# Performance work log

Measured on AMD Instinct MI355X. Metric: run time of the kernel, lower is better.

The kernel has to match this reference:

```python
import jax, jax.numpy as jnp
import numpy as np

N_IN, N_OUT, K, G = 128, 256, 3, 3  # G = grid intervals (setup hard-codes 3)
KNOT_LO, KNOT_HI = -1.0, 1.0


def make_grid(n, k, G, lo=KNOT_LO, hi=KNOT_HI):
    # Augmented knot vector: G+1 knots extended by k on each side -> G+2k+1 points
    h = (hi - lo) / G
    g = jnp.arange(-k, G + k + 1, dtype=jnp.float32) * h + lo
    return jnp.tile(g[None, :], (n, 1))  # (n, G+2k+1)


def get_spline_basis(x, grid, k):
    # Cox-de Boor recursion. x: (batch, n); grid: (n, G+2k+1)
    g = grid[None, :, :]          # (1, n, G+2k+1)
    xx = x[:, :, None]            # (batch, n, 1)
    # order-0 (indicator) basis: (batch, n, G+2k)
    basis = ((xx >= g[..., :-1]) & (xx < g[..., 1:])).astype(x.dtype)
    for kk in range(1, k + 1):
        left = (xx - g[..., : -(kk + 1)]) / (g[..., kk:-1] - g[..., : -(kk + 1)]) * basis[..., :-1]
        right = (g[..., kk + 1 :] - xx) / (g[..., kk + 1 :] - g[..., 1:-kk]) * basis[..., 1:]
        basis = left + right
    return basis  # (batch, n, G+k)


def setup_inputs() -> dict:
    key = jax.random.key(0)
    k1, k2 = jax.random.split(key)
    batch = 512
    n = N_IN * N_OUT
    x = jax.random.normal(k1, (batch, N_IN), dtype=jnp.float32)
    grid = make_grid(n, K, G)                                        # state (non-trainable)
    c_basis = 0.1 * jax.random.normal(k2, (n, G + K), dtype=jnp.float32)
    c_spl = jnp.ones((n,), dtype=jnp.float32)
    c_res = jnp.ones((n,), dtype=jnp.float32)
    return {"x": x, "grid": grid, "c_basis": c_basis, "c_spl": c_spl, "c_res": c_res}


def reference(x, grid, c_basis, c_spl, c_res):
    batch = x.shape[0]
    # Broadcast each input node to every output edge, out-major ordering:
    # einsum('ij,k->ikj', x, ones(n_out)).reshape(batch, n_in*n_out)
    x_ext = jnp.broadcast_to(x[:, None, :], (batch, N_OUT, N_IN)).reshape(batch, N_OUT * N_IN)
    # residual branch: swish, transposed to (n, batch)
    res = jax.nn.swish(x_ext).T
    # spline branch: (batch, n, G+K) basis combined with per-edge coeffs -> (n, batch)
    Bi = get_spline_basis(x_ext, grid, K)
    spl = jnp.einsum('ij,bij->ib', c_basis, Bi)
    y = c_spl[:, None] * spl + c_res[:, None] * res            # (n, batch)
    y = y.reshape(N_OUT, N_IN, batch).sum(axis=1) / N_IN       # (n_out, batch)
    return y.T                                                 # (batch, n_out)
```

## Files before the change

### kernel.cpp

```cpp
#include <hip/hip_runtime.h>
#include <hip/hip_bf16.h>


typedef short short8 __attribute__((ext_vector_type(8)));
typedef float f32x4 __attribute__((ext_vector_type(4)));

static __device__ inline unsigned short bf16_bits(float f) {
    union { __hip_bfloat16 h; unsigned short u; } cvt;
    cvt.h = __float2bfloat16(f);
    return cvt.u;
}

__global__ __launch_bounds__(256) void build_fw(
    const float* __restrict__ x,
    const float* __restrict__ grid,
    const float* __restrict__ c_basis,
    const float* __restrict__ c_spl,
    const float* __restrict__ c_res,
    unsigned short* __restrict__ F,
    unsigned short* __restrict__ W)
{
    const int tid = blockIdx.x * 256 + threadIdx.x;

    if (tid < 512 * 128) {
        const float t0    = grid[0];
        const float inv_h = 1.0f / (grid[1] - grid[0]);

        const float xv = x[tid];
        const float u  = (xv - t0) * inv_h;

        float d[10];
#pragma unroll
        for (int s = 0; s < 10; ++s) d[s] = u - (float)s;

        float I0[9];
#pragma unroll
        for (int s = 0; s < 9; ++s)
            I0[s] = (d[s] >= 0.0f && d[s + 1] < 0.0f) ? 1.0f : 0.0f;

        float b1[8];
#pragma unroll
        for (int s = 0; s < 8; ++s)
            b1[s] = d[s] * I0[s] - d[s + 2] * I0[s + 1];

        float b2[7];
#pragma unroll
        for (int s = 0; s < 7; ++s)
            b2[s] = d[s] * b1[s] - d[s + 3] * b1[s + 1];

        float b3[6];
#pragma unroll
        for (int s = 0; s < 6; ++s)
            b3[s] = (d[s] * b2[s] - d[s + 4] * b2[s + 1]) * (1.0f / 6.0f);

        const float e  = __expf(-xv);
        const float sw = xv * __builtin_amdgcn_rcpf(1.0f + e);

        short8 v;
        v[0] = bf16_bits(b3[0]);
        v[1] = bf16_bits(b3[1]);
        v[2] = bf16_bits(b3[2]);
        v[3] = bf16_bits(b3[3]);
        v[4] = bf16_bits(b3[4]);
        v[5] = bf16_bits(b3[5]);
        v[6] = bf16_bits(sw);
        v[7] = 0;
        *(short8*)(F + tid * 8) = v;
    } else if (tid < 512 * 128 + 32768) {
        const int j = tid - 512 * 128;
        const float spl = c_spl[j];
        const float* cbp = c_basis + j * 6;

        short8 v;
        v[0] = bf16_bits(spl * cbp[0]);
        v[1] = bf16_bits(spl * cbp[1]);
        v[2] = bf16_bits(spl * cbp[2]);
        v[3] = bf16_bits(spl * cbp[3]);
        v[4] = bf16_bits(spl * cbp[4]);
        v[5] = bf16_bits(spl * cbp[5]);
        v[6] = bf16_bits(c_res[j]);
        v[7] = 0;
        *(short8*)(W + j * 8) = v;
    }
}

__global__ __launch_bounds__(64) void kan_gemm(
    const unsigned short* __restrict__ F,
    const unsigned short* __restrict__ W,
    float* __restrict__ out)
{
    const int bt   = blockIdx.x >> 4;
    const int ot   = blockIdx.x & 15;
    const int lane = threadIdx.x;
    const int r    = lane & 15;
    const int q    = lane >> 4;

    const unsigned short* fp = F + (bt * 16 + r) * 1024 + q * 8;
    const unsigned short* wp = W + (ot * 16 + r) * 1024 + q * 8;

    f32x4 acc = {0.0f, 0.0f, 0.0f, 0.0f};

#pragma unroll
    for (int k0 = 0; k0 < 1024; k0 += 128) {
        short8 a0 = *(const short8*)(fp + k0);
        short8 a1 = *(const short8*)(fp + k0 + 32);
        short8 a2 = *(const short8*)(fp + k0 + 64);
        short8 a3 = *(const short8*)(fp + k0 + 96);
        short8 w0 = *(const short8*)(wp + k0);
        short8 w1 = *(const short8*)(wp + k0 + 32);
        short8 w2 = *(const short8*)(wp + k0 + 64);
        short8 w3 = *(const short8*)(wp + k0 + 96);
        acc = __builtin_amdgcn_mfma_f32_16x16x32_bf16(a0, w0, acc, 0, 0, 0);
        acc = __builtin_amdgcn_mfma_f32_16x16x32_bf16(a1, w1, acc, 0, 0, 0);
        acc = __builtin_amdgcn_mfma_f32_16x16x32_bf16(a2, w2, acc, 0, 0, 0);
        acc = __builtin_amdgcn_mfma_f32_16x16x32_bf16(a3, w3, acc, 0, 0, 0);
    }

    const float scale = 1.0f / 128.0f;
    const int   orow  = bt * 16 + q * 4;
    const int   ocol  = ot * 16 + r;
#pragma unroll
    for (int reg = 0; reg < 4; ++reg)
        out[(orow + reg) * 256 + ocol] = acc[reg] * scale;
}

extern "C" void kernel_launch(void* const* d_in, const int* in_sizes, int n_in,
                              void* d_out, int out_size, void* d_ws, size_t ws_size,
                              hipStream_t stream) {
    const float* x       = (const float*)d_in[0];
    const float* grid    = (const float*)d_in[1];
    const float* c_basis = (const float*)d_in[2];
    const float* c_spl   = (const float*)d_in[3];
    const float* c_res   = (const float*)d_in[4];
    float* out = (float*)d_out;

    unsigned short* F = (unsigned short*)d_ws;
    unsigned short* W = (unsigned short*)((char*)d_ws + 512 * 1024 * 2);

    build_fw<<<384, 256, 0, stream>>>(x, grid, c_basis, c_spl, c_res, F, W);
    kan_gemm<<<512, 64, 0, stream>>>(F, W, out);
}
```

Baseline: 67.65 us.

## Fuse feature/weight build into MFMA GEMM via swizzled LDS tiles

Merges the basis/weight construction kernel and the GEMM kernel into one. Each block computes its 16x1024 feature tile and 16x1024 weight tile directly into XOR-swizzled shared memory, splits K across four waves, and reduces the partial sums through LDS. This removes the global workspace round trip and one launch. In exchange, basis and weight construction is recomputed redundantly across blocks and uses 64KB of LDS per block.

New measurement: 66.55 us. Within noise of the previous version (-1.6%).

```diff
diff --git a/kernel.cpp b/kernel.cpp
--- a/kernel.cpp
+++ b/kernel.cpp
@@ -11,50 +11,58 @@
     return cvt.u;
 }
 
-__global__ __launch_bounds__(256) void build_fw(
+__global__ __launch_bounds__(256) void kan_fused(
     const float* __restrict__ x,
     const float* __restrict__ grid,
     const float* __restrict__ c_basis,
     const float* __restrict__ c_spl,
     const float* __restrict__ c_res,
-    unsigned short* __restrict__ F,
-    unsigned short* __restrict__ W)
+    float* __restrict__ out)
 {
-    const int tid = blockIdx.x * 256 + threadIdx.x;
+    __shared__ short8 lds_v[4096];
+    unsigned char* lds = (unsigned char*)lds_v;
 
-    if (tid < 512 * 128) {
-        const float t0    = grid[0];
-        const float inv_h = 1.0f / (grid[1] - grid[0]);
+    const int bt = blockIdx.x >> 4;
+    const int ot = blockIdx.x & 15;
+    const int t  = threadIdx.x;
 
-        const float xv = x[tid];
+    const float t0    = grid[0];
+    const float inv_h = 1.0f / (grid[1] - grid[0]);
+
+    for (int s = 0; s < 8; ++s) {
+        const int e  = s * 256 + t;
+        const int bl = e >> 7;
+        const int i  = e & 127;
+
+        const float xv = x[(bt * 16 + bl) * 128 + i];
         const float u  = (xv - t0) * inv_h;
 
         float d[10];
 #pragma unroll
-        for (int s = 0; s < 10; ++s) d[s] = u - (float)s;
+        for (int m = 0; m < 10; ++m) d[m] = u - (float)m;
 
         float I0[9];
 #pragma unroll
-        for (int s = 0; s < 9; ++s)
-            I0[s] = (d[s] >= 0.0f && d[s + 1] < 0.0f) ? 1.0f : 0.0f;
+        for (int m = 0; m < 9; ++m)
+            I0[m] = (d[m] >= 0.0f && d[m + 1] < 0.0f) ? 1.0f : 0.0f;
 
         float b1[8];
 #pragma unroll
-        for (int s = 0; s < 8; ++s)
-            b1[s] = d[s] * I0[s] - d[s + 2] * I0[s + 1];
+        for (int m = 0; m < 8; ++m)
+            b1[m] = d[m] * I0[m] - d[m + 2] * I0[m + 1];
 
         float b2[7];
 #pragma unroll
-        for (int s = 0; s < 7; ++s)
-            b2[s] = d[s] * b1[s] - d[s + 3] * b1[s + 1];
+        for (int m = 0; m < 7; ++m)
+            b2[m] = d[m] * b1[m] - d[m + 3] * b1[m + 1];
 
         float b3[6];
 #pragma unroll
-        for (int s = 0; s < 6; ++s)
-            b3[s] = (d[s] * b2[s] - d[s + 4] * b2[s + 1]) * (1.0f / 6.0f);
+        for (int m = 0; m < 6; ++m)
+            b3[m] = (d[m] * b2[m] - d[m + 4] * b2[m + 1]) * (1.0f / 6.0f);
 
-        const float e  = __expf(-xv);
-        const float sw = xv * __builtin_amdgcn_rcpf(1.0f + e);
+        const float e_  = __expf(-xv);
+        const float sw  = xv * __builtin_amdgcn_rcpf(1.0f + e_);
 
         short8 v;
         v[0] = bf16_bits(b3[0]);
@@ -65,10 +73,16 @@
         v[5] = bf16_bits(b3[5]);
         v[6] = bf16_bits(sw);
         v[7] = 0;
-        *(short8*)(F + tid * 8) = v;
-    } else if (tid < 512 * 128 + 32768) {
-        const int j = tid - 512 * 128;
-        const float spl = c_spl[j];
+        *(short8*)(lds + bl * 2048 + ((i * 16) ^ ((bl & 7) << 4))) = v;
+    }
+
+    for (int s = 0; s < 8; ++s) {
+        const int e  = s * 256 + t;
+        const int ol = e >> 7;
+        const int i  = e & 127;
+        const int j  = (ot * 16 + ol) * 128 + i;
+
+        const float  spl = c_spl[j];
         const float* cbp = c_basis + j * 6;
 
         short8 v;
@@ -80,48 +94,48 @@
         v[5] = bf16_bits(spl * cbp[5]);
         v[6] = bf16_bits(c_res[j]);
         v[7] = 0;
-        *(short8*)(W + j * 8) = v;
+        *(short8*)(lds + 32768 + ol * 2048 + ((i * 16) ^ ((ol & 7) << 4))) = v;
     }
-}
 
-__global__ __launch_bounds__(64) void kan_gemm(
-    const unsigned short* __restrict__ F,
-    const unsigned short* __restrict__ W,
-    float* __restrict__ out)
-{
-    const int bt   = blockIdx.x >> 4;
-    const int ot   = blockIdx.x & 15;
-    const int lane = threadIdx.x;
+    __syncthreads();
+
+    const int wv   = t >> 6;
+    const int lane = t & 63;
     const int r    = lane & 15;
     const int q    = lane >> 4;
+    const int xr   = (r & 7) << 4;
 
-    const unsigned short* fp = F + (bt * 16 + r) * 1024 + q * 8;
-    const unsigned short* wp = W + (ot * 16 + r) * 1024 + q * 8;
+    const unsigned char* Fb = lds + r * 2048;
+    const unsigned char* Wb = lds + 32768 + r * 2048;
 
     f32x4 acc = {0.0f, 0.0f, 0.0f, 0.0f};
-
 #pragma unroll
-    for (int k0 = 0; k0 < 1024; k0 += 128) {
-        short8 a0 = *(const short8*)(fp + k0);
-        short8 a1 = *(const short8*)(fp + k0 + 32);
-        short8 a2 = *(const short8*)(fp + k0 + 64);
-        short8 a3 = *(const short8*)(fp + k0 + 96);
-        short8 w0 = *(const short8*)(wp + k0);
-        short8 w1 = *(const short8*)(wp + k0 + 32);
-        short8 w2 = *(const short8*)(wp + k0 + 64);
-        short8 w3 = *(const short8*)(wp + k0 + 96);
-        acc = __builtin_amdgcn_mfma_f32_16x16x32_bf16(a0, w0, acc, 0, 0, 0);
-        acc = __builtin_amdgcn_mfma_f32_16x16x32_bf16(a1, w1, acc, 0, 0, 0);
-        acc = __builtin_amdgcn_mfma_f32_16x16x32_bf16(a2, w2, acc, 0, 0, 0);
-        acc = __builtin_amdgcn_mfma_f32_16x16x32_bf16(a3, w3, acc, 0, 0, 0);
+    for (int cc = 0; cc < 8; ++cc) {
+        const int c   = wv * 8 + cc;
+        const int off = (c * 64 + q * 16) ^ xr;
+        short8 a = *(const short8*)(Fb + off);
+        short8 b = *(const short8*)(Wb + off);
+        acc = __builtin_amdgcn_mfma_f32_16x16x32_bf16(a, b, acc, 0, 0, 0);
     }
 
-    const float scale = 1.0f / 128.0f;
-    const int   orow  = bt * 16 + q * 4;
-    const int   ocol  = ot * 16 + r;
+    __syncthreads();
+    *(f32x4*)(lds + t * 16) = acc;
+    __syncthreads();
+
+    if (t < 64) {
+        f32x4 s0 = *(const f32x4*)(lds + t * 16);
+        f32x4 s1 = *(const f32x4*)(lds + (64 + t) * 16);
+        f32x4 s2 = *(const f32x4*)(lds + (128 + t) * 16);
+        f32x4 s3 = *(const f32x4*)(lds + (192 + t) * 16);
+        f32x4 sum = (s0 + s1) + (s2 + s3);
+
+        const float scale = 1.0f / 128.0f;
+        const int   orow  = bt * 16 + (t >> 4) * 4;
+        const int   ocol  = ot * 16 + (t & 15);
 #pragma unroll
-    for (int reg = 0; reg < 4; ++reg)
-        out[(orow + reg) * 256 + ocol] = acc[reg] * scale;
+        for (int reg = 0; reg < 4; ++reg)
+            out[(orow + reg) * 256 + ocol] = sum[reg] * scale;
+    }
 }
 
 extern "C" void kernel_launch(void* const* d_in, const int* in_sizes, int n_in,
@@ -134,9 +148,5 @@
     const float* c_res   = (const float*)d_in[4];
     float* out = (float*)d_out;
 
-    unsigned short* F = (unsigned short*)d_ws;
-    unsigned short* W = (unsigned short*)((char*)d_ws + 512 * 1024 * 2);
-
-    build_fw<<<384, 256, 0, stream>>>(x, grid, c_basis, c_spl, c_res, F, W);
-    kan_gemm<<<512, 64, 0, stream>>>(F, W, out);
+    kan_fused<<<512, 256, 0, stream>>>(x, grid, c_basis, c_spl, c_res, out);
 }
```
